# Performance work log

Measured on AMD Instinct MI355X. Metric: run time of the kernel, lower is better.

Reference implementation:

```python
import jax, jax.numpy as jnp
import numpy as np

N = 100000
E = 1600000
D = 128


def setup_inputs() -> dict:
    key = jax.random.key(0)
    ks = jax.random.split(key, 8)
    x = jax.random.normal(ks[0], (N, D), dtype=jnp.float32)
    edge_index = jax.random.randint(ks[1], (2, E), 0, N, dtype=jnp.int64)
    # Xavier-uniform linear weights, zero-ish biases (PyTorch default bias is uniform; keep small random)
    def xavier(k, fan_in, fan_out):
        limit = float(np.sqrt(6.0 / (fan_in + fan_out)))
        return jax.random.uniform(k, (fan_out, fan_in), minval=-limit, maxval=limit, dtype=jnp.float32)
    W1 = xavier(ks[2], D, D); b1 = jnp.zeros((D,), jnp.float32)
    W2 = xavier(ks[3], D, D); b2 = jnp.zeros((D,), jnp.float32)
    W3 = xavier(ks[4], D, D); b3 = jnp.zeros((D,), jnp.float32)
    return {"x": x, "edge_index": edge_index, "W1": W1, "b1": b1,
            "W2": W2, "b2": b2, "W3": W3, "b3": b3}


def reference(x, edge_index, W1, b1, W2, b2, W3, b3):
    n = x.shape[0]
    loop = jnp.arange(n, dtype=edge_index.dtype)
    row = jnp.concatenate([edge_index[0], loop])  # source (x_j index)
    col = jnp.concatenate([edge_index[1], loop])  # target (aggregation index)
    # degree over row after self-loops; every node appears at least once
    deg = jax.ops.segment_sum(jnp.ones_like(row, dtype=x.dtype), row, num_segments=n)
    dis = deg ** -0.5
    norm = dis[row] * dis[col]  # [E+N]

    def gconv(h, W, b):
        h = h @ W.T + b                      # linear projection [N, D]
        msg = norm[:, None] * h[row]         # gather + elementwise norm [E+N, D]
        return jax.ops.segment_sum(msg, col, num_segments=n)  # scatter-add

    h = jax.nn.relu(gconv(x, W1, b1))
    h = jax.nn.relu(gconv(h, W2, b2))
    h = jax.nn.relu(gconv(h, W3, b3))
    return h
```

## Files before the change

### kernel.cpp

```cpp
#include <hip/hip_runtime.h>
#include <hip/hip_fp16.h>

#define THREADS 256
#define ELL 64
#define EPT 4

typedef _Float16 f16x8 __attribute__((ext_vector_type(8)));
typedef float f32x4 __attribute__((ext_vector_type(4)));

__device__ inline uint2 pack_half4(float4 v) {
    __half2 a = __floats2half2_rn(v.x, v.y);
    __half2 b = __floats2half2_rn(v.z, v.w);
    uint2 o;
    o.x = *reinterpret_cast<unsigned int*>(&a);
    o.y = *reinterpret_cast<unsigned int*>(&b);
    return o;
}
__device__ inline float4 unpack_half4(uint2 v) {
    __half2 a = *reinterpret_cast<__half2*>(&v.x);
    __half2 b = *reinterpret_cast<__half2*>(&v.y);
    float2 f0 = __half22float2(a);
    float2 f1 = __half22float2(b);
    return make_float4(f0.x, f0.y, f1.x, f1.y);
}


__global__ void detect_kernel(const int* __restrict__ ei, int* __restrict__ flag) {
    if (blockIdx.x == 0 && threadIdx.x == 0) {
        int nz = 0;
        for (int i = 1; i < 256; i += 2) nz |= ei[i];
        *flag = (nz == 0) ? 1 : 0;
    }
}

__global__ void preinit_kernel(int* __restrict__ deg, int* __restrict__ fill,
                               int* __restrict__ csr, int n) {
    int i = blockIdx.x * blockDim.x + threadIdx.x;
    if (i < n) {
        deg[i] = 1;
        fill[i] = 1;
        csr[(size_t)i * ELL] = i;
    }
}

__global__ void edge_kernel(const int* __restrict__ ei, const int* __restrict__ flag,
                            int* __restrict__ deg, int* __restrict__ fill,
                            int* __restrict__ csr, int eN) {
    const int t = blockIdx.x * blockDim.x + threadIdx.x;
    const int base = t * EPT;
    if (base >= eN) return;
    int r[EPT], c[EPT];
    const int m = min(EPT, eN - base);
    if (*flag) {
        const long long* e64 = (const long long*)ei;
#pragma unroll
        for (int k = 0; k < EPT; ++k) {
            if (k < m) { r[k] = (int)e64[base + k]; c[k] = (int)e64[eN + base + k]; }
        }
    } else {
#pragma unroll
        for (int k = 0; k < EPT; ++k) {
            if (k < m) { r[k] = ei[base + k]; c[k] = ei[eN + base + k]; }
        }
    }
#pragma unroll
    for (int k = 0; k < EPT; ++k)
        if (k < m) atomicAdd(&deg[r[k]], 1);
    int pos[EPT];
#pragma unroll
    for (int k = 0; k < EPT; ++k)
        if (k < m) pos[k] = atomicAdd(&fill[c[k]], 1);
#pragma unroll
    for (int k = 0; k < EPT; ++k)
        if (k < m) csr[(size_t)c[k] * ELL + pos[k]] = r[k];
}

__global__ void dis_kernel(const int* __restrict__ deg, float* __restrict__ dis, int n) {
    int i = blockIdx.x * blockDim.x + threadIdx.x;
    if (i < n) dis[i] = 1.0f / sqrtf((float)deg[i]);
}

__global__ void sumw_kernel(const int* __restrict__ csr, const int* __restrict__ fill,
                            const float* __restrict__ dis, float* __restrict__ sumw,
                            float* __restrict__ w32, int n) {
    int i = blockIdx.x * blockDim.x + threadIdx.x;
    if (i >= n) return;
    int len = fill[i];
    const int base = i * ELL;
    const float dg = dis[i];
    float t = 0.f;
    for (int j = 0; j < len; ++j) {
        float w = dg * dis[csr[base + j]];
        w32[base + j] = w;
        t += w;
    }
    sumw[i] = t;
}

__global__ void tofp16_kernel(const float4* __restrict__ x, uint2* __restrict__ o, int total) {
    int i = blockIdx.x * blockDim.x + threadIdx.x;
    if (i < total) o[i] = pack_half4(x[i]);
}

__global__ void wfrag_kernel(const float* __restrict__ w0, const float* __restrict__ w1,
                             const float* __restrict__ w2, _Float16* __restrict__ wf) {
    int i = blockIdx.x * blockDim.x + threadIdx.x;
    if (i >= 3 * 8 * 4 * 64) return;
    int lane = i & 63;
    int kt = (i >> 6) & 3;
    int nt = (i >> 8) & 7;
    int l  = i >> 11;
    const float* w = (l == 0) ? w0 : (l == 1) ? w1 : w2;
    int o  = nt * 16 + (lane & 15);
    int kb = kt * 32 + (lane >> 4) * 8;
    _Float16* dst = wf + (size_t)i * 8;
#pragma unroll
    for (int j = 0; j < 8; ++j) dst[j] = (_Float16)w[o * 128 + kb + j];
}


__global__ void agg_kernel(const uint2* __restrict__ h, const int* __restrict__ csr,
                           const int* __restrict__ fill, const float* __restrict__ w32,
                           uint2* __restrict__ out, int n) {
    const int wid = blockIdx.x * (blockDim.x >> 6) + (threadIdx.x >> 6);
    const int lane = threadIdx.x & 63;
    const int half = lane >> 5;
    const int l32 = lane & 31;
    if (wid >= n) return;
    const int len = fill[wid];
    const int base = wid * ELL;

    float4 a0 = make_float4(0.f, 0.f, 0.f, 0.f);
    float4 a1 = make_float4(0.f, 0.f, 0.f, 0.f);
    int j = half;
    for (; j + 2 < len; j += 4) {
        int u0 = csr[base + j];
        int u1 = csr[base + j + 2];
        float w0 = w32[base + j];
        float w1 = w32[base + j + 2];
        float4 v0 = unpack_half4(h[(size_t)u0 * 32 + l32]);
        float4 v1 = unpack_half4(h[(size_t)u1 * 32 + l32]);
        a0.x = fmaf(w0, v0.x, a0.x); a0.y = fmaf(w0, v0.y, a0.y);
        a0.z = fmaf(w0, v0.z, a0.z); a0.w = fmaf(w0, v0.w, a0.w);
        a1.x = fmaf(w1, v1.x, a1.x); a1.y = fmaf(w1, v1.y, a1.y);
        a1.z = fmaf(w1, v1.z, a1.z); a1.w = fmaf(w1, v1.w, a1.w);
    }
    if (j < len) {
        int u = csr[base + j];
        float w = w32[base + j];
        float4 v = unpack_half4(h[(size_t)u * 32 + l32]);
        a0.x = fmaf(w, v.x, a0.x); a0.y = fmaf(w, v.y, a0.y);
        a0.z = fmaf(w, v.z, a0.z); a0.w = fmaf(w, v.w, a0.w);
    }
    a0.x += a1.x; a0.y += a1.y; a0.z += a1.z; a0.w += a1.w;

    a0.x += __shfl_xor(a0.x, 32, 64);
    a0.y += __shfl_xor(a0.y, 32, 64);
    a0.z += __shfl_xor(a0.z, 32, 64);
    a0.w += __shfl_xor(a0.w, 32, 64);

    if (half == 0) {
        out[(size_t)wid * 32 + l32] = pack_half4(a0);
    }
}

template <bool OUT16>
__global__ __launch_bounds__(THREADS) void lin_mfma_kernel(
    const _Float16* __restrict__ a16, const _Float16* __restrict__ wfrag,
    const float* __restrict__ bias, const float* __restrict__ sumw,
    float* __restrict__ outf, _Float16* __restrict__ outh, int n) {
    const int lane = threadIdx.x & 63;
    const int g = lane >> 4;
    const int m15 = lane & 15;
    const int wavesPerBlock = blockDim.x >> 6;
    const int wave = blockIdx.x * wavesPerBlock + (threadIdx.x >> 6);
    const int nwaves = gridDim.x * wavesPerBlock;

    f16x8 wf[8][4];
#pragma unroll
    for (int nt = 0; nt < 8; ++nt)
#pragma unroll
        for (int kt = 0; kt < 4; ++kt)
            wf[nt][kt] = *reinterpret_cast<const f16x8*>(
                wfrag + ((size_t)((nt * 4 + kt) * 64 + lane)) * 8);

    const int ntiles = (n + 15) >> 4;
    for (int t = wave; t < ntiles; t += nwaves) {
        const int myrow = t * 16 + m15;
        const int rr = (myrow < n) ? myrow : (n - 1);
        const _Float16* arow = a16 + (size_t)rr * 128 + g * 8;
        f16x8 af[4];
#pragma unroll
        for (int kt = 0; kt < 4; ++kt)
            af[kt] = *reinterpret_cast<const f16x8*>(arow + kt * 32);

        f32x4 acc[8];
#pragma unroll
        for (int nt = 0; nt < 8; ++nt) acc[nt] = (f32x4){0.f, 0.f, 0.f, 0.f};
#pragma unroll
        for (int kt = 0; kt < 4; ++kt)
#pragma unroll
            for (int nt = 0; nt < 8; ++nt)
                acc[nt] = __builtin_amdgcn_mfma_f32_16x16x32_f16(
                    wf[nt][kt], af[kt], acc[nt], 0, 0, 0);

        if (myrow < n) {
            const float sw = sumw[myrow];
#pragma unroll
            for (int nt = 0; nt < 8; ++nt) {
                const float4 b4 = *reinterpret_cast<const float4*>(bias + nt * 16 + g * 4);
                float vx = fmaxf(acc[nt][0] + sw * b4.x, 0.f);
                float vy = fmaxf(acc[nt][1] + sw * b4.y, 0.f);
                float vz = fmaxf(acc[nt][2] + sw * b4.z, 0.f);
                float vw = fmaxf(acc[nt][3] + sw * b4.w, 0.f);
                size_t oidx = (size_t)myrow * 128 + nt * 16 + g * 4;
                if (OUT16) {
                    *reinterpret_cast<uint2*>(outh + oidx) =
                        pack_half4(make_float4(vx, vy, vz, vw));
                } else {
                    *reinterpret_cast<float4*>(outf + oidx) =
                        make_float4(vx, vy, vz, vw);
                }
            }
        }
    }
}


extern "C" void kernel_launch(void* const* d_in, const int* in_sizes, int n_in,
                              void* d_out, int out_size, void* d_ws, size_t ws_size,
                              hipStream_t stream) {
    const float* x  = (const float*)d_in[0];
    const int*   ei = (const int*)d_in[1];
    const float* Ws[3] = {(const float*)d_in[2], (const float*)d_in[4], (const float*)d_in[6]};
    const float* bs[3] = {(const float*)d_in[3], (const float*)d_in[5], (const float*)d_in[7]};
    const int n = in_sizes[0] / 128;
    const int e = in_sizes[1] / 2;

    char* ws = (char*)d_ws;
    size_t cur = 0;
    auto alloc = [&](size_t bytes) {
        void* p = ws + cur;
        cur = (cur + bytes + 255) & ~(size_t)255;
        return p;
    };
    uint2*     A16  = (uint2*)alloc((size_t)n * 128 * 2);
    uint2*     H16  = (uint2*)alloc((size_t)n * 128 * 2);
    int*       csr  = (int*)  alloc((size_t)n * ELL * 4);
    float*     w32  = (float*)alloc((size_t)n * ELL * 4);
    int*       deg  = (int*)  alloc((size_t)n * 4);
    int*       fill = (int*)  alloc((size_t)n * 4);
    float*     dis  = (float*)alloc((size_t)n * 4);
    float*     sumw = (float*)alloc((size_t)n * 4);
    _Float16*  wf   = (_Float16*)alloc(3 * 8 * 4 * 64 * 8 * 2);
    int*       flag = (int*)  alloc(4);

    detect_kernel<<<1, 64, 0, stream>>>(ei, flag);
    preinit_kernel<<<(n + 255) / 256, 256, 0, stream>>>(deg, fill, csr, n);
    edge_kernel<<<((e + EPT - 1) / EPT + 255) / 256, 256, 0, stream>>>(
        ei, flag, deg, fill, csr, e);
    dis_kernel<<<(n + 255) / 256, 256, 0, stream>>>(deg, dis, n);
    sumw_kernel<<<(n + 255) / 256, 256, 0, stream>>>(csr, fill, dis, sumw, w32, n);
    tofp16_kernel<<<(n * 32 + 255) / 256, 256, 0, stream>>>((const float4*)x, H16, n * 32);
    wfrag_kernel<<<(6144 + 255) / 256, 256, 0, stream>>>(Ws[0], Ws[1], Ws[2], wf);

    for (int l = 0; l < 3; ++l) {
        agg_kernel<<<(n + 3) / 4, 256, 0, stream>>>(
            H16, csr, fill, w32, A16, n);
        const _Float16* wfl = wf + (size_t)l * 8 * 4 * 64 * 8;
        if (l < 2) {
            lin_mfma_kernel<true><<<512, THREADS, 0, stream>>>(
                (const _Float16*)A16, wfl, bs[l], sumw,
                nullptr, (_Float16*)H16, n);
        } else {
            lin_mfma_kernel<false><<<512, THREADS, 0, stream>>>(
                (const _Float16*)A16, wfl, bs[l], sumw,
                (float*)d_out, nullptr, n);
        }
    }
}
```

Before: 482.3 us.

## Compute degrees via LDS-sliced histogram and unroll aggregation loop to four accumulators

Source-degree counting moves out of the edge kernel's global atomics into a separate kernel. Each block builds a shared-memory histogram over one node range and one edge slice, and dis_kernel sums the per-slice partials. This removes 1.6M contended global atomics, but every histogram block rescans its whole edge slice, so the edge rows are read about eight times over. Separately, the aggregation loop is unrolled to four independent accumulators so more gathers are in flight per wave.

```diff
diff --git a/kernel.cpp b/kernel.cpp
--- a/kernel.cpp
+++ b/kernel.cpp
@@ -4,6 +4,8 @@
 #define THREADS 256
 #define ELL 64
 #define EPT 4
+#define RSIZE 13000
+#define NSLICE 8
 
 typedef _Float16 f16x8 __attribute__((ext_vector_type(8)));
 typedef float f32x4 __attribute__((ext_vector_type(4)));
@@ -33,19 +35,50 @@
     }
 }
 
-__global__ void preinit_kernel(int* __restrict__ deg, int* __restrict__ fill,
-                               int* __restrict__ csr, int n) {
+__global__ void preinit_kernel(int* __restrict__ fill, int* __restrict__ csr, int n) {
     int i = blockIdx.x * blockDim.x + threadIdx.x;
     if (i < n) {
-        deg[i] = 1;
         fill[i] = 1;
         csr[(size_t)i * ELL] = i;
     }
 }
 
+__global__ __launch_bounds__(THREADS) void deghist_kernel(
+    const int* __restrict__ ei, const int* __restrict__ flag,
+    int* __restrict__ ghist, int eN, int n, int nr) {
+    __shared__ int lh[RSIZE];
+    const int g = blockIdx.x / NSLICE;
+    const int s = blockIdx.x % NSLICE;
+    const int tid = threadIdx.x;
+    for (int i = tid; i < RSIZE; i += THREADS) lh[i] = 0;
+    __syncthreads();
+
+    const int lo = (int)((long long)eN * s / NSLICE);
+    const int hi = (int)((long long)eN * (s + 1) / NSLICE);
+    const int rbase = g * RSIZE;
+    if (*flag) {
+        const long long* e64 = (const long long*)ei;
+        for (int idx = lo + tid; idx < hi; idx += THREADS) {
+            int r = (int)e64[idx];
+            unsigned int local = (unsigned int)(r - rbase);
+            if (local < RSIZE) atomicAdd(&lh[local], 1);
+        }
+    } else {
+        for (int idx = lo + tid; idx < hi; idx += THREADS) {
+            int r = ei[idx];
+            unsigned int local = (unsigned int)(r - rbase);
+            if (local < RSIZE) atomicAdd(&lh[local], 1);
+        }
+    }
+    __syncthreads();
+    for (int i = tid; i < RSIZE; i += THREADS) {
+        int node = rbase + i;
+        if (node < n) ghist[(size_t)s * n + node] = lh[i];
+    }
+}
+
 __global__ void edge_kernel(const int* __restrict__ ei, const int* __restrict__ flag,
-                            int* __restrict__ deg, int* __restrict__ fill,
-                            int* __restrict__ csr, int eN) {
+                            int* __restrict__ fill, int* __restrict__ csr, int eN) {
     const int t = blockIdx.x * blockDim.x + threadIdx.x;
     const int base = t * EPT;
     if (base >= eN) return;
@@ -54,18 +87,13 @@
     if (*flag) {
         const long long* e64 = (const long long*)ei;
 #pragma unroll
-        for (int k = 0; k < EPT; ++k) {
+        for (int k = 0; k < EPT; ++k)
             if (k < m) { r[k] = (int)e64[base + k]; c[k] = (int)e64[eN + base + k]; }
-        }
     } else {
 #pragma unroll
-        for (int k = 0; k < EPT; ++k) {
+        for (int k = 0; k < EPT; ++k)
             if (k < m) { r[k] = ei[base + k]; c[k] = ei[eN + base + k]; }
-        }
-    }
-#pragma unroll
-    for (int k = 0; k < EPT; ++k)
-        if (k < m) atomicAdd(&deg[r[k]], 1);
+    }
     int pos[EPT];
 #pragma unroll
     for (int k = 0; k < EPT; ++k)
@@ -75,9 +103,13 @@
         if (k < m) csr[(size_t)c[k] * ELL + pos[k]] = r[k];
 }
 
-__global__ void dis_kernel(const int* __restrict__ deg, float* __restrict__ dis, int n) {
-    int i = blockIdx.x * blockDim.x + threadIdx.x;
-    if (i < n) dis[i] = 1.0f / sqrtf((float)deg[i]);
+__global__ void dis_kernel(const int* __restrict__ ghist, float* __restrict__ dis, int n) {
+    int i = blockIdx.x * blockDim.x + threadIdx.x;
+    if (i >= n) return;
+    int deg = 1;
+#pragma unroll
+    for (int s = 0; s < NSLICE; ++s) deg += ghist[(size_t)s * n + i];
+    dis[i] = 1.0f / sqrtf((float)deg);
 }
 
 __global__ void sumw_kernel(const int* __restrict__ csr, const int* __restrict__ fill,
@@ -132,27 +164,42 @@
 
     float4 a0 = make_float4(0.f, 0.f, 0.f, 0.f);
     float4 a1 = make_float4(0.f, 0.f, 0.f, 0.f);
+    float4 a2 = make_float4(0.f, 0.f, 0.f, 0.f);
+    float4 a3 = make_float4(0.f, 0.f, 0.f, 0.f);
     int j = half;
-    for (; j + 2 < len; j += 4) {
+    for (; j + 6 < len; j += 8) {
         int u0 = csr[base + j];
         int u1 = csr[base + j + 2];
+        int u2 = csr[base + j + 4];
+        int u3 = csr[base + j + 6];
         float w0 = w32[base + j];
         float w1 = w32[base + j + 2];
+        float w2 = w32[base + j + 4];
+        float w3 = w32[base + j + 6];
         float4 v0 = unpack_half4(h[(size_t)u0 * 32 + l32]);
         float4 v1 = unpack_half4(h[(size_t)u1 * 32 + l32]);
+        float4 v2 = unpack_half4(h[(size_t)u2 * 32 + l32]);
+        float4 v3 = unpack_half4(h[(size_t)u3 * 32 + l32]);
         a0.x = fmaf(w0, v0.x, a0.x); a0.y = fmaf(w0, v0.y, a0.y);
         a0.z = fmaf(w0, v0.z, a0.z); a0.w = fmaf(w0, v0.w, a0.w);
         a1.x = fmaf(w1, v1.x, a1.x); a1.y = fmaf(w1, v1.y, a1.y);
         a1.z = fmaf(w1, v1.z, a1.z); a1.w = fmaf(w1, v1.w, a1.w);
-    }
-    if (j < len) {
+        a2.x = fmaf(w2, v2.x, a2.x); a2.y = fmaf(w2, v2.y, a2.y);
+        a2.z = fmaf(w2, v2.z, a2.z); a2.w = fmaf(w2, v2.w, a2.w);
+        a3.x = fmaf(w3, v3.x, a3.x); a3.y = fmaf(w3, v3.y, a3.y);
+        a3.z = fmaf(w3, v3.z, a3.z); a3.w = fmaf(w3, v3.w, a3.w);
+    }
+    for (; j < len; j += 2) {
         int u = csr[base + j];
         float w = w32[base + j];
         float4 v = unpack_half4(h[(size_t)u * 32 + l32]);
         a0.x = fmaf(w, v.x, a0.x); a0.y = fmaf(w, v.y, a0.y);
         a0.z = fmaf(w, v.z, a0.z); a0.w = fmaf(w, v.w, a0.w);
     }
-    a0.x += a1.x; a0.y += a1.y; a0.z += a1.z; a0.w += a1.w;
+    a0.x += a1.x + a2.x + a3.x;
+    a0.y += a1.y + a2.y + a3.y;
+    a0.z += a1.z + a2.z + a3.z;
+    a0.w += a1.w + a2.w + a3.w;
 
     a0.x += __shfl_xor(a0.x, 32, 64);
     a0.y += __shfl_xor(a0.y, 32, 64);
@@ -244,22 +291,25 @@
         cur = (cur + bytes + 255) & ~(size_t)255;
         return p;
     };
-    uint2*     A16  = (uint2*)alloc((size_t)n * 128 * 2);
-    uint2*     H16  = (uint2*)alloc((size_t)n * 128 * 2);
-    int*       csr  = (int*)  alloc((size_t)n * ELL * 4);
-    float*     w32  = (float*)alloc((size_t)n * ELL * 4);
-    int*       deg  = (int*)  alloc((size_t)n * 4);
-    int*       fill = (int*)  alloc((size_t)n * 4);
-    float*     dis  = (float*)alloc((size_t)n * 4);
-    float*     sumw = (float*)alloc((size_t)n * 4);
-    _Float16*  wf   = (_Float16*)alloc(3 * 8 * 4 * 64 * 8 * 2);
-    int*       flag = (int*)  alloc(4);
+    uint2*     A16   = (uint2*)alloc((size_t)n * 128 * 2);
+    uint2*     H16   = (uint2*)alloc((size_t)n * 128 * 2);
+    int*       csr   = (int*)  alloc((size_t)n * ELL * 4);
+    float*     w32   = (float*)alloc((size_t)n * ELL * 4);
+    int*       ghist = (int*)  alloc((size_t)NSLICE * n * 4);
+    int*       fill  = (int*)  alloc((size_t)n * 4);
+    float*     dis   = (float*)alloc((size_t)n * 4);
+    float*     sumw  = (float*)alloc((size_t)n * 4);
+    _Float16*  wf    = (_Float16*)alloc(3 * 8 * 4 * 64 * 8 * 2);
+    int*       flag  = (int*)  alloc(4);
+
+    const int nr = (n + RSIZE - 1) / RSIZE;
 
     detect_kernel<<<1, 64, 0, stream>>>(ei, flag);
-    preinit_kernel<<<(n + 255) / 256, 256, 0, stream>>>(deg, fill, csr, n);
+    preinit_kernel<<<(n + 255) / 256, 256, 0, stream>>>(fill, csr, n);
+    deghist_kernel<<<nr * NSLICE, THREADS, 0, stream>>>(ei, flag, ghist, e, n, nr);
     edge_kernel<<<((e + EPT - 1) / EPT + 255) / 256, 256, 0, stream>>>(
-        ei, flag, deg, fill, csr, e);
-    dis_kernel<<<(n + 255) / 256, 256, 0, stream>>>(deg, dis, n);
+        ei, flag, fill, csr, e);
+    dis_kernel<<<(n + 255) / 256, 256, 0, stream>>>(ghist, dis, n);
     sumw_kernel<<<(n + 255) / 256, 256, 0, stream>>>(csr, fill, dis, sumw, w32, n);
     tofp16_kernel<<<(n * 32 + 255) / 256, 256, 0, stream>>>((const float4*)x, H16, n * 32);
     wfrag_kernel<<<(6144 + 255) / 256, 256, 0, stream>>>(Ws[0], Ws[1], Ws[2], wf);
```

Measured after the change: 648.9 us. +34.5%, slower.
